# Kernel optimization log

Measured on AMD Instinct MI355X. Metric: run time of the kernel, lower is better.

The kernel has to match this reference:

```python
import jax, jax.numpy as jnp
import numpy as np

D, H, O, E, N = 1024, 2048, 1024, 8, 4096

def setup_inputs() -> dict:
    key = jax.random.key(0)
    ks = jax.random.split(key, 5)
    scale = lambda fan_in: 1.0 / np.sqrt(fan_in)
    x = jax.random.normal(ks[0], (N, D), dtype=jnp.float32)
    Wr = jax.random.normal(ks[1], (E, D), dtype=jnp.float32) * scale(D)
    br = jnp.zeros((E,), dtype=jnp.float32)
    W1 = jax.random.normal(ks[2], (E, H, D), dtype=jnp.float32) * scale(D)
    b1 = jnp.zeros((E, H), dtype=jnp.float32)
    W2 = jax.random.normal(ks[3], (E, O, H), dtype=jnp.float32) * scale(H)
    b2 = jnp.zeros((E, O), dtype=jnp.float32)
    return {"x": x, "Wr": Wr, "br": br, "W1": W1, "b1": b1, "W2": W2, "b2": b2}

def reference(x, Wr, br, W1, b1, W2, b2):
    # router softmax over experts: [N, E]
    route = jax.nn.softmax(x @ Wr.T + br, axis=-1)
    # all experts as one grouped GEMM: hidden [N, E, H]
    h = jnp.einsum('nd,ehd->neh', x, W1) + b1
    h = jnp.square(jax.nn.relu(h))  # squared ReLU
    # expert outputs [N, E, O]
    y = jnp.einsum('neh,eoh->neo', h, W2) + b2
    # softmax-weighted combine over experts -> [N, O]
    return jnp.einsum('ne,neo->no', route, y)
```

## Files before the change

### kernel.cpp

```cpp
#include <hip/hip_runtime.h>
#include <hip/hip_bf16.h>
#include <stdint.h>

#define Dd 1024
#define Hd 2048
#define Od 1024
#define Ed 8
#define Nd 4096

typedef __bf16 bf16x8 __attribute__((ext_vector_type(8)));
typedef float f32x4 __attribute__((ext_vector_type(4)));

__device__ __forceinline__ void gload16(const void* g, void* l) {
  __builtin_amdgcn_global_load_lds(
      (const __attribute__((address_space(1))) void*)g,
      (__attribute__((address_space(3))) void*)l, 16, 0, 0);
}

__device__ __forceinline__ unsigned short f2bf(float f) {
  __hip_bfloat16 h = __float2bfloat16(f);
  return *reinterpret_cast<unsigned short*>(&h);
}

__global__ void cvt_kernel(const float* __restrict__ in,
                           unsigned short* __restrict__ out, int ngroups) {
  int stride = gridDim.x * blockDim.x;
  for (int g = blockIdx.x * blockDim.x + threadIdx.x; g < ngroups; g += stride) {
    const float4* p = (const float4*)(in + (size_t)g * 8);
    float4 a = p[0], b = p[1];
    unsigned short o[8];
    o[0] = f2bf(a.x); o[1] = f2bf(a.y); o[2] = f2bf(a.z); o[3] = f2bf(a.w);
    o[4] = f2bf(b.x); o[5] = f2bf(b.y); o[6] = f2bf(b.z); o[7] = f2bf(b.w);
    *(int4*)(out + (size_t)g * 8) = *(int4*)o;
  }
}

__global__ void router_kernel(const float* __restrict__ x, const float* __restrict__ Wr,
                              const float* __restrict__ br, float* __restrict__ route) {
  const int n = blockIdx.x;
  const int t = threadIdx.x;
  __shared__ float xs[Dd];
  #pragma unroll
  for (int i = 0; i < Dd / 256; ++i) xs[t + i * 256] = x[(size_t)n * Dd + t + i * 256];
  __syncthreads();
  float p[Ed];
  #pragma unroll
  for (int e = 0; e < Ed; ++e) p[e] = 0.f;
  for (int d = t; d < Dd; d += 256) {
    float xv = xs[d];
    #pragma unroll
    for (int e = 0; e < Ed; ++e) p[e] += xv * Wr[e * Dd + d];
  }
  __shared__ float red[Ed][4];
  const int lane = t & 63, wid = t >> 6;
  #pragma unroll
  for (int e = 0; e < Ed; ++e) {
    float v = p[e];
    for (int off = 32; off > 0; off >>= 1) v += __shfl_down(v, off);
    if (lane == 0) red[e][wid] = v;
  }
  __syncthreads();
  if (t == 0) {
    float lg[Ed], mx = -1e30f;
    #pragma unroll
    for (int e = 0; e < Ed; ++e) {
      lg[e] = red[e][0] + red[e][1] + red[e][2] + red[e][3] + br[e];
      mx = fmaxf(mx, lg[e]);
    }
    float s = 0.f;
    #pragma unroll
    for (int e = 0; e < Ed; ++e) { lg[e] = expf(lg[e] - mx); s += lg[e]; }
    float inv = 1.f / s;
    #pragma unroll
    for (int e = 0; e < Ed; ++e) route[(size_t)n * Ed + e] = lg[e] * inv;
  }
}

__global__ void init_out_kernel(const float* __restrict__ route, const float* __restrict__ b2,
                                float* __restrict__ out) {
  const int idx = blockIdx.x * 256 + threadIdx.x;
  const int n = idx >> 10, o = idx & (Od - 1);
  float s = 0.f;
  #pragma unroll
  for (int e = 0; e < Ed; ++e) s += route[(size_t)n * Ed + e] * b2[e * Od + o];
  out[idx] = s;
}

#define LGKM0 do { asm volatile("s_waitcnt lgkmcnt(0)" ::: "memory"); \
                   __builtin_amdgcn_sched_barrier(0); } while (0)

template <int MODE>
__global__ __launch_bounds__(512, 2) void gemm8p(
    const unsigned short* __restrict__ Ag,
    const unsigned short* __restrict__ Bg,
    const float* __restrict__ bias,
    const float* __restrict__ route,
    void* __restrict__ Cout,
    int n0, int ncRows, int ngx) {
  extern __shared__ unsigned short smem[];
  unsigned short* As = smem;
  unsigned short* Bs = smem + 32768;

  const int nwg = gridDim.x;
  const int orig = blockIdx.x;
  const int q8 = nwg >> 3;
  const int wg = (orig & 7) * q8 + (orig >> 3);
  const int bx = wg % ngx;
  const int rem = wg / ngx;
  int by, ez;
  if (MODE == 0) { by = rem & 7; ez = rem >> 3; }
  else           { by = rem & 3; ez = rem >> 2; }

  const int tid = threadIdx.x;
  const int wid = tid >> 6, lane = tid & 63;
  const int wm = wid >> 2, wn = wid & 3;

  const int trow = tid >> 3;
  const int tcs = ((tid & 7) ^ (trow & 7)) * 8;

  const int NT = (MODE == 0) ? (Dd / 64) : (2 * Hd / 64);

  auto stageA = [&](int buf, int kt, int mh) {
    #pragma unroll
    for (int s = 0; s < 2; ++s) {
      const int pa = mh * 128 + s * 64 + trow;
      const int m = ((pa >> 6) & 1) * 128 + ((pa >> 7) & 1) * 64 + (pa & 63);
      const unsigned short* g;
      if (MODE == 0) {
        g = Ag + (size_t)(n0 + bx * 256 + m) * Dd + kt * 64 + tcs;
      } else {
        const int e = ez * 2 + (kt >> 5);
        g = Ag + (size_t)e * ncRows * Hd + (size_t)(bx * 256 + m) * Hd + (kt & 31) * 64 + tcs;
      }
      gload16(g, &As[(size_t)buf * 16384 + (size_t)(mh * 128 + s * 64) * 64 + wid * 512]);
    }
  };
  auto stageB = [&](int buf, int kt, int nh) {
    #pragma unroll
    for (int s = 0; s < 2; ++s) {
      const int pb = nh * 128 + s * 64 + trow;
      const int n = ((pb >> 5) & 3) * 64 + ((pb >> 7) & 1) * 32 + (pb & 31);
      const unsigned short* g;
      if (MODE == 0) {
        g = Bg + (size_t)ez * Hd * Dd + (size_t)(by * 256 + n) * Dd + kt * 64 + tcs;
      } else {
        const int e = ez * 2 + (kt >> 5);
        g = Bg + (size_t)e * Od * Hd + (size_t)(by * 256 + n) * Hd + (kt & 31) * 64 + tcs;
      }
      gload16(g, &Bs[(size_t)buf * 16384 + (size_t)(nh * 128 + s * 64) * 64 + wid * 512]);
    }
  };

  const int laneRow = lane & 15;
  const int swzc[2] = { ((lane >> 4) ^ (lane & 7)) << 3,
                        (((lane >> 4) + 4) ^ (lane & 7)) << 3 };
  const int aRowBase = (wm * 64 + laneRow) * 64;
  const int bRowBase = (wn * 32 + laneRow) * 64;

  auto rdA = [&](int buf, int mh, int mi, int kk) -> bf16x8 {
    const int addr = buf * 16384 + aRowBase + (mh * 128 + mi * 16) * 64 + swzc[kk];
    return *(const bf16x8*)&As[addr];
  };
  auto rdB = [&](int buf, int nh, int ni, int kk) -> bf16x8 {
    const int addr = buf * 16384 + bRowBase + (nh * 128 + ni * 16) * 64 + swzc[kk];
    return *(const bf16x8*)&Bs[addr];
  };

  f32x4 acc[8][4];
  #pragma unroll
  for (int i = 0; i < 8; ++i)
    #pragma unroll
    for (int j = 0; j < 4; ++j) acc[i][j] = (f32x4){0.f, 0.f, 0.f, 0.f};
  bf16x8 a0[4][2], a1[4][2], b0[2][2], b1[2][2];

  stageB(0, 0, 0); stageA(0, 0, 1); stageA(0, 0, 0); stageB(0, 0, 1);
  stageB(1, 1, 0); stageA(1, 1, 1);
  asm volatile("s_waitcnt vmcnt(4)" ::: "memory");
  __builtin_amdgcn_sched_barrier(0);
  __builtin_amdgcn_s_barrier();

  for (int U = 0; U < NT; ++U) {
    const int buf = U & 1, nbuf = buf ^ 1;
    #pragma unroll
    for (int mi = 0; mi < 4; ++mi) { a0[mi][0] = rdA(buf, 0, mi, 0); a0[mi][1] = rdA(buf, 0, mi, 1); }
    #pragma unroll
    for (int ni = 0; ni < 2; ++ni) { b0[ni][0] = rdB(buf, 0, ni, 0); b0[ni][1] = rdB(buf, 0, ni, 1); }
    if (U + 1 < NT) stageA(nbuf, U + 1, 0);
    __builtin_amdgcn_s_barrier();
    LGKM0;
    __builtin_amdgcn_s_setprio(1);
    #pragma unroll
    for (int mi = 0; mi < 4; ++mi)
      #pragma unroll
      for (int ni = 0; ni < 2; ++ni) {
        acc[mi][ni] = __builtin_amdgcn_mfma_f32_16x16x32_bf16(a0[mi][0], b0[ni][0], acc[mi][ni], 0, 0, 0);
        acc[mi][ni] = __builtin_amdgcn_mfma_f32_16x16x32_bf16(a0[mi][1], b0[ni][1], acc[mi][ni], 0, 0, 0);
      }
    __builtin_amdgcn_s_setprio(0);
    __builtin_amdgcn_s_barrier();
    #pragma unroll
    for (int mi = 0; mi < 4; ++mi) { a1[mi][0] = rdA(buf, 1, mi, 0); a1[mi][1] = rdA(buf, 1, mi, 1); }
    if (U + 1 < NT) stageB(nbuf, U + 1, 1);
    __builtin_amdgcn_s_barrier();
    LGKM0;
    __builtin_amdgcn_s_setprio(1);
    #pragma unroll
    for (int mi = 0; mi < 4; ++mi)
      #pragma unroll
      for (int ni = 0; ni < 2; ++ni) {
        acc[4 + mi][ni] = __builtin_amdgcn_mfma_f32_16x16x32_bf16(a1[mi][0], b0[ni][0], acc[4 + mi][ni], 0, 0, 0);
        acc[4 + mi][ni] = __builtin_amdgcn_mfma_f32_16x16x32_bf16(a1[mi][1], b0[ni][1], acc[4 + mi][ni], 0, 0, 0);
      }
    __builtin_amdgcn_s_setprio(0);
    __builtin_amdgcn_s_barrier();
    #pragma unroll
    for (int ni = 0; ni < 2; ++ni) { b1[ni][0] = rdB(buf, 1, ni, 0); b1[ni][1] = rdB(buf, 1, ni, 1); }
    if (U + 2 < NT) stageB(buf, U + 2, 0);
    __builtin_amdgcn_s_barrier();
    LGKM0;
    __builtin_amdgcn_s_setprio(1);
    #pragma unroll
    for (int mi = 0; mi < 4; ++mi)
      #pragma unroll
      for (int ni = 0; ni < 2; ++ni) {
        acc[4 + mi][2 + ni] = __builtin_amdgcn_mfma_f32_16x16x32_bf16(a1[mi][0], b1[ni][0], acc[4 + mi][2 + ni], 0, 0, 0);
        acc[4 + mi][2 + ni] = __builtin_amdgcn_mfma_f32_16x16x32_bf16(a1[mi][1], b1[ni][1], acc[4 + mi][2 + ni], 0, 0, 0);
      }
    __builtin_amdgcn_s_setprio(0);
    __builtin_amdgcn_s_barrier();
    if (U + 2 < NT) stageA(buf, U + 2, 1);
    __builtin_amdgcn_s_barrier();
    __builtin_amdgcn_s_setprio(1);
    #pragma unroll
    for (int mi = 0; mi < 4; ++mi)
      #pragma unroll
      for (int ni = 0; ni < 2; ++ni) {
        acc[mi][2 + ni] = __builtin_amdgcn_mfma_f32_16x16x32_bf16(a0[mi][0], b1[ni][0], acc[mi][2 + ni], 0, 0, 0);
        acc[mi][2 + ni] = __builtin_amdgcn_mfma_f32_16x16x32_bf16(a0[mi][1], b1[ni][1], acc[mi][2 + ni], 0, 0, 0);
      }
    __builtin_amdgcn_s_setprio(0);
    if (U + 2 < NT) {
      asm volatile("s_waitcnt vmcnt(4)" ::: "memory");
    } else if (U + 1 < NT) {
      asm volatile("s_waitcnt vmcnt(0)" ::: "memory");
    }
    __builtin_amdgcn_sched_barrier(0);
    __builtin_amdgcn_s_barrier();
  }

  if (MODE == 0) {
    unsigned short* hs = (unsigned short*)Cout;
    unsigned short* base = hs + (size_t)ez * ((size_t)ncRows * Hd);
    #pragma unroll
    for (int M = 0; M < 8; ++M) {
      const int mh = M >> 2, mi = M & 3;
      const int row = bx * 256 + wm * 128 + mh * 64 + mi * 16 + (lane >> 4) * 4;
      float rw[4];
      #pragma unroll
      for (int j = 0; j < 4; ++j) rw[j] = route[(size_t)(n0 + row + j) * Ed + ez];
      #pragma unroll
      for (int N = 0; N < 4; ++N) {
        const int nh = N >> 1, ni = N & 1;
        const int col = by * 256 + wn * 64 + nh * 32 + ni * 16 + (lane & 15);
        const float bv = bias[ez * Hd + col];
        #pragma unroll
        for (int j = 0; j < 4; ++j) {
          float v = acc[M][N][j] + bv;
          v = fmaxf(v, 0.f);
          v = v * v * rw[j];
          base[(size_t)(row + j) * Hd + col] = f2bf(v);
        }
      }
    }
  } else {
    float* out = (float*)Cout;
    #pragma unroll
    for (int M = 0; M < 8; ++M) {
      const int mh = M >> 2, mi = M & 3;
      const int row = n0 + bx * 256 + wm * 128 + mh * 64 + mi * 16 + (lane >> 4) * 4;
      #pragma unroll
      for (int N = 0; N < 4; ++N) {
        const int nh = N >> 1, ni = N & 1;
        const int col = by * 256 + wn * 64 + nh * 32 + ni * 16 + (lane & 15);
        #pragma unroll
        for (int j = 0; j < 4; ++j)
          atomicAdd(out + (size_t)(row + j) * Od + col, acc[M][N][j]);
      }
    }
  }
}

extern "C" void kernel_launch(void* const* d_in, const int* in_sizes, int n_in,
                              void* d_out, int out_size, void* d_ws, size_t ws_size,
                              hipStream_t stream) {
  const float* x  = (const float*)d_in[0];
  const float* Wr = (const float*)d_in[1];
  const float* br = (const float*)d_in[2];
  const float* W1 = (const float*)d_in[3];
  const float* b1 = (const float*)d_in[4];
  const float* W2 = (const float*)d_in[5];
  const float* b2 = (const float*)d_in[6];
  float* out = (float*)d_out;

  char* ws = (char*)d_ws;
  size_t off = 0;
  float* route = (float*)(ws + off);                 off += (size_t)Nd * Ed * 4;
  unsigned short* xb  = (unsigned short*)(ws + off); off += (size_t)Nd * Dd * 2;
  unsigned short* w1b = (unsigned short*)(ws + off); off += (size_t)Ed * Hd * Dd * 2;
  unsigned short* w2b = (unsigned short*)(ws + off); off += (size_t)Ed * Od * Hd * 2;
  unsigned short* hs  = (unsigned short*)(ws + off);

  size_t remain = (ws_size > off) ? (ws_size - off) : 0;
  const size_t perRow = (size_t)Ed * Hd * 2;
  long long ncMax = (long long)(remain / perRow);
  int NC = (int)(ncMax & ~255LL);
  if (NC > Nd) NC = Nd;
  if (NC < 256) NC = 256;

  hipFuncSetAttribute(reinterpret_cast<const void*>(&gemm8p<0>),
                      hipFuncAttributeMaxDynamicSharedMemorySize, 131072);
  hipFuncSetAttribute(reinterpret_cast<const void*>(&gemm8p<1>),
                      hipFuncAttributeMaxDynamicSharedMemorySize, 131072);

  cvt_kernel<<<1024, 256, 0, stream>>>(x, xb, Nd * Dd / 8);
  cvt_kernel<<<2048, 256, 0, stream>>>(W1, w1b, Ed * Hd * Dd / 8);
  cvt_kernel<<<2048, 256, 0, stream>>>(W2, w2b, Ed * Od * Hd / 8);
  router_kernel<<<Nd, 256, 0, stream>>>(x, Wr, br, route);
  init_out_kernel<<<Nd * Od / 256, 256, 0, stream>>>(route, b2, out);

  for (int n0 = 0; n0 < Nd; n0 += NC) {
    int nc = (NC < (Nd - n0)) ? NC : (Nd - n0);
    int ngx = nc / 256;
    gemm8p<0><<<ngx * 8 * Ed, 512, 131072, stream>>>(xb, w1b, b1, route, hs, n0, nc, ngx);
    gemm8p<1><<<ngx * 4 * 4, 512, 131072, stream>>>(hs, w2b, nullptr, nullptr, out, n0, nc, ngx);
  }
}
```

Measured before the change: 368.6 us.

## Split second GEMM per expert, fuse x conversion into router, restructure prefetch

```diff
diff --git a/kernel.cpp b/kernel.cpp
--- a/kernel.cpp
+++ b/kernel.cpp
@@ -36,12 +36,15 @@
 }
 
 __global__ void router_kernel(const float* __restrict__ x, const float* __restrict__ Wr,
-                              const float* __restrict__ br, float* __restrict__ route) {
+                              const float* __restrict__ br, float* __restrict__ route,
+                              unsigned short* __restrict__ xb) {
   const int n = blockIdx.x;
   const int t = threadIdx.x;
   __shared__ float xs[Dd];
-  #pragma unroll
-  for (int i = 0; i < Dd / 256; ++i) xs[t + i * 256] = x[(size_t)n * Dd + t + i * 256];
+  float4 v = *(const float4*)&x[(size_t)n * Dd + t * 4];
+  *(float4*)&xs[t * 4] = v;
+  unsigned short o[4] = {f2bf(v.x), f2bf(v.y), f2bf(v.z), f2bf(v.w)};
+  *(uint2*)&xb[(size_t)n * Dd + t * 4] = *(const uint2*)o;
   __syncthreads();
   float p[Ed];
   #pragma unroll
@@ -55,9 +58,9 @@
   const int lane = t & 63, wid = t >> 6;
   #pragma unroll
   for (int e = 0; e < Ed; ++e) {
-    float v = p[e];
-    for (int off = 32; off > 0; off >>= 1) v += __shfl_down(v, off);
-    if (lane == 0) red[e][wid] = v;
+    float vv = p[e];
+    for (int off = 32; off > 0; off >>= 1) vv += __shfl_down(vv, off);
+    if (lane == 0) red[e][wid] = vv;
   }
   __syncthreads();
   if (t == 0) {
@@ -118,7 +121,7 @@
   const int trow = tid >> 3;
   const int tcs = ((tid & 7) ^ (trow & 7)) * 8;
 
-  const int NT = (MODE == 0) ? (Dd / 64) : (2 * Hd / 64);
+  const int NT = (MODE == 0) ? (Dd / 64) : (Hd / 64);
 
   auto stageA = [&](int buf, int kt, int mh) {
     #pragma unroll
@@ -129,8 +132,7 @@
       if (MODE == 0) {
         g = Ag + (size_t)(n0 + bx * 256 + m) * Dd + kt * 64 + tcs;
       } else {
-        const int e = ez * 2 + (kt >> 5);
-        g = Ag + (size_t)e * ncRows * Hd + (size_t)(bx * 256 + m) * Hd + (kt & 31) * 64 + tcs;
+        g = Ag + (size_t)ez * ncRows * Hd + (size_t)(bx * 256 + m) * Hd + kt * 64 + tcs;
       }
       gload16(g, &As[(size_t)buf * 16384 + (size_t)(mh * 128 + s * 64) * 64 + wid * 512]);
     }
@@ -144,8 +146,7 @@
       if (MODE == 0) {
         g = Bg + (size_t)ez * Hd * Dd + (size_t)(by * 256 + n) * Dd + kt * 64 + tcs;
       } else {
-        const int e = ez * 2 + (kt >> 5);
-        g = Bg + (size_t)e * Od * Hd + (size_t)(by * 256 + n) * Hd + (kt & 31) * 64 + tcs;
+        g = Bg + (size_t)ez * Od * Hd + (size_t)(by * 256 + n) * Hd + kt * 64 + tcs;
       }
       gload16(g, &Bs[(size_t)buf * 16384 + (size_t)(nh * 128 + s * 64) * 64 + wid * 512]);
     }
@@ -173,19 +174,19 @@
     for (int j = 0; j < 4; ++j) acc[i][j] = (f32x4){0.f, 0.f, 0.f, 0.f};
   bf16x8 a0[4][2], a1[4][2], b0[2][2], b1[2][2];
 
-  stageB(0, 0, 0); stageA(0, 0, 1); stageA(0, 0, 0); stageB(0, 0, 1);
-  stageB(1, 1, 0); stageA(1, 1, 1);
-  asm volatile("s_waitcnt vmcnt(4)" ::: "memory");
+  stageA(0, 0, 0); stageB(0, 0, 0); stageA(0, 0, 1); stageB(0, 0, 1);
+  stageA(1, 1, 0); stageB(1, 1, 0); stageA(1, 1, 1); stageB(1, 1, 1);
+  asm volatile("s_waitcnt vmcnt(8)" ::: "memory");
   __builtin_amdgcn_sched_barrier(0);
   __builtin_amdgcn_s_barrier();
 
   for (int U = 0; U < NT; ++U) {
-    const int buf = U & 1, nbuf = buf ^ 1;
+    const int buf = U & 1;
+    const bool pf = (U + 2 < NT);
     #pragma unroll
     for (int mi = 0; mi < 4; ++mi) { a0[mi][0] = rdA(buf, 0, mi, 0); a0[mi][1] = rdA(buf, 0, mi, 1); }
     #pragma unroll
     for (int ni = 0; ni < 2; ++ni) { b0[ni][0] = rdB(buf, 0, ni, 0); b0[ni][1] = rdB(buf, 0, ni, 1); }
-    if (U + 1 < NT) stageA(nbuf, U + 1, 0);
     __builtin_amdgcn_s_barrier();
     LGKM0;
     __builtin_amdgcn_s_setprio(1);
@@ -200,7 +201,7 @@
     __builtin_amdgcn_s_barrier();
     #pragma unroll
     for (int mi = 0; mi < 4; ++mi) { a1[mi][0] = rdA(buf, 1, mi, 0); a1[mi][1] = rdA(buf, 1, mi, 1); }
-    if (U + 1 < NT) stageB(nbuf, U + 1, 1);
+    if (pf) { stageA(buf, U + 2, 0); stageB(buf, U + 2, 0); }
     __builtin_amdgcn_s_barrier();
     LGKM0;
     __builtin_amdgcn_s_setprio(1);
@@ -215,7 +216,7 @@
     __builtin_amdgcn_s_barrier();
     #pragma unroll
     for (int ni = 0; ni < 2; ++ni) { b1[ni][0] = rdB(buf, 1, ni, 0); b1[ni][1] = rdB(buf, 1, ni, 1); }
-    if (U + 2 < NT) stageB(buf, U + 2, 0);
+    if (pf) stageA(buf, U + 2, 1);
     __builtin_amdgcn_s_barrier();
     LGKM0;
     __builtin_amdgcn_s_setprio(1);
@@ -228,7 +229,7 @@
       }
     __builtin_amdgcn_s_setprio(0);
     __builtin_amdgcn_s_barrier();
-    if (U + 2 < NT) stageA(buf, U + 2, 1);
+    if (pf) stageB(buf, U + 2, 1);
     __builtin_amdgcn_s_barrier();
     __builtin_amdgcn_s_setprio(1);
     #pragma unroll
@@ -239,8 +240,8 @@
         acc[mi][2 + ni] = __builtin_amdgcn_mfma_f32_16x16x32_bf16(a0[mi][1], b1[ni][1], acc[mi][2 + ni], 0, 0, 0);
       }
     __builtin_amdgcn_s_setprio(0);
-    if (U + 2 < NT) {
-      asm volatile("s_waitcnt vmcnt(4)" ::: "memory");
+    if (pf) {
+      asm volatile("s_waitcnt vmcnt(8)" ::: "memory");
     } else if (U + 1 < NT) {
       asm volatile("s_waitcnt vmcnt(0)" ::: "memory");
     }
@@ -322,16 +323,15 @@
   hipFuncSetAttribute(reinterpret_cast<const void*>(&gemm8p<1>),
                       hipFuncAttributeMaxDynamicSharedMemorySize, 131072);
 
-  cvt_kernel<<<1024, 256, 0, stream>>>(x, xb, Nd * Dd / 8);
   cvt_kernel<<<2048, 256, 0, stream>>>(W1, w1b, Ed * Hd * Dd / 8);
   cvt_kernel<<<2048, 256, 0, stream>>>(W2, w2b, Ed * Od * Hd / 8);
-  router_kernel<<<Nd, 256, 0, stream>>>(x, Wr, br, route);
+  router_kernel<<<Nd, 256, 0, stream>>>(x, Wr, br, route, xb);
   init_out_kernel<<<Nd * Od / 256, 256, 0, stream>>>(route, b2, out);
 
   for (int n0 = 0; n0 < Nd; n0 += NC) {
     int nc = (NC < (Nd - n0)) ? NC : (Nd - n0);
     int ngx = nc / 256;
     gemm8p<0><<<ngx * 8 * Ed, 512, 131072, stream>>>(xb, w1b, b1, route, hs, n0, nc, ngx);
-    gemm8p<1><<<ngx * 4 * 4, 512, 131072, stream>>>(hs, w2b, nullptr, nullptr, out, n0, nc, ngx);
-  }
-}
+    gemm8p<1><<<ngx * 4 * Ed, 512, 131072, stream>>>(hs, w2b, nullptr, nullptr, out, n0, nc, ngx);
+  }
+}
```

New measurement: 426.8 us. 15.8% more time.
